# Optimization experiments

Hardware: AMD Instinct MI355X
Metric: run time of the kernel (lower is better)

The kernel has to match this reference:

```python
import jax, jax.numpy as jnp
import numpy as np

H = 1.0                 # grid spacing (init kwarg h)
SRC = (48, 48, 48)      # source grid index = round((x,y,z)/h)
N_ITER = 288
BIG = 1e5               # large-but-finite 'infinity' (keeps gradients NaN-free)


def _godunov_step(u, f):
    """One Jacobi-parallel Godunov upwind update of |grad u| = f on a cubic grid."""
    up = jnp.pad(u, 1, constant_values=BIG)
    # upwind neighbor minima along each axis
    a = jnp.minimum(up[:-2, 1:-1, 1:-1], up[2:, 1:-1, 1:-1])
    b = jnp.minimum(up[1:-1, :-2, 1:-1], up[1:-1, 2:, 1:-1])
    c = jnp.minimum(up[1:-1, 1:-1, :-2], up[1:-1, 1:-1, 2:])
    # sort (a,b,c) -> lo <= mid <= hi
    lo = jnp.minimum(jnp.minimum(a, b), c)
    hi = jnp.maximum(jnp.maximum(a, b), c)
    mid = a + b + c - lo - hi
    fh = f * H
    # 1D candidate
    u1 = lo + fh
    # 2D candidate: (lo+mid+sqrt(2 fh^2 - (lo-mid)^2))/2, guarded sqrt
    d2 = 2.0 * fh * fh - (lo - mid) ** 2
    u2 = jnp.where(d2 > 0, 0.5 * (lo + mid + jnp.sqrt(jnp.where(d2 > 0, d2, 1.0))), BIG)
    # 3D candidate: root of 3 t^2 - 2 s t + (q - fh^2) = 0
    s = lo + mid + hi
    d3 = s * s - 3.0 * (lo * lo + mid * mid + hi * hi - fh * fh)
    u3 = jnp.where(d3 > 0, (s + jnp.sqrt(jnp.where(d3 > 0, d3, 1.0))) / 3.0, BIG)
    cand = jnp.where(u1 <= mid, u1, jnp.where(u2 <= hi, u2, u3))
    un = jnp.minimum(u, cand)          # monotone update (causality)
    return un.at[SRC].set(0.0)         # pin source travel time


def setup_inputs() -> dict:
    key = jax.random.key(0)
    # slowness field, bounded away from zero (velocities in [2/3, 2])
    f = 0.5 + jax.random.uniform(key, (96, 96, 96), dtype=jnp.float32)
    return {"f": f}


def reference(f):
    u0 = jnp.full(f.shape, BIG, dtype=f.dtype).at[SRC].set(0.0)
    step = jax.checkpoint(lambda u, _: (_godunov_step(u, f), None))
    u, _ = jax.lax.scan(step, u0, None, length=N_ITER)
    return u
```

## Files before the change

kernel.cpp:

```cpp
#include <hip/hip_runtime.h>


#define N   96
#define N2  (96 * 96)
#define N3  (96 * 96 * 96)
#define BIGV 1e5f
#define SRC_IDX (48 * N2 + 48 * N + 48)

__global__ __launch_bounds__(256) void eik_init(float* __restrict__ u) {
    int idx = blockIdx.x * 256 + threadIdx.x;
    u[idx] = (idx == SRC_IDX) ? 0.0f : BIGV;
}

__global__ __launch_bounds__(256) void eik_step(const float* __restrict__ u,
                                                const float* __restrict__ f,
                                                float* __restrict__ un) {
    int idx = blockIdx.x * 256 + threadIdx.x;
    int k = idx % N;
    int t = idx / N;
    int j = t % N;
    int i = t / N;

    float uc = u[idx];

    float xm = (i > 0)     ? u[idx - N2] : BIGV;
    float xp = (i < N - 1) ? u[idx + N2] : BIGV;
    float ym = (j > 0)     ? u[idx - N]  : BIGV;
    float yp = (j < N - 1) ? u[idx + N]  : BIGV;
    float zm = (k > 0)     ? u[idx - 1]  : BIGV;
    float zp = (k < N - 1) ? u[idx + 1]  : BIGV;

    float a = fminf(xm, xp);
    float b = fminf(ym, yp);
    float c = fminf(zm, zp);

    float lo  = fminf(fminf(a, b), c);
    float hi  = fmaxf(fmaxf(a, b), c);
    float mid = a + b + c - lo - hi;

    float fh = f[idx];

    float u1 = lo + fh;

    float dlm = lo - mid;
    float d2  = 2.0f * fh * fh - dlm * dlm;
    float u2  = (d2 > 0.0f) ? 0.5f * (lo + mid + sqrtf(d2)) : BIGV;

    float s  = lo + mid + hi;
    float q  = lo * lo + mid * mid + hi * hi - fh * fh;
    float d3 = s * s - 3.0f * q;
    float u3 = (d3 > 0.0f) ? (s + sqrtf(d3)) / 3.0f : BIGV;

    float cand = (u1 <= mid) ? u1 : ((u2 <= hi) ? u2 : u3);
    float unv  = fminf(uc, cand);

    if (idx == SRC_IDX) unv = 0.0f;
    un[idx] = unv;
}

extern "C" void kernel_launch(void* const* d_in, const int* in_sizes, int n_in,
                              void* d_out, int out_size, void* d_ws, size_t ws_size,
                              hipStream_t stream) {
    const float* f = (const float*)d_in[0];
    float* A = (float*)d_out;
    float* B = (float*)d_ws;

    const int nblk = N3 / 256;

    eik_init<<<nblk, 256, 0, stream>>>(A);

    for (int it = 0; it < 288; ++it) {
        const float* src = (it & 1) ? B : A;
        float*       dst = (it & 1) ? A : B;
        eik_step<<<nblk, 256, 0, stream>>>(src, f, dst);
    }
}
```

Before: 1.937 ms.

## Fuse four Jacobi sweeps per launch with LDS temporal blocking and halos

Each block loads a 12^3 tile plus a 4-cell halo into shared memory and performs four Godunov sweeps in LDS with shrinking valid regions before writing the tile back. This cuts kernel launches and global memory round-trips by a factor of four. It also skips the quadratic solve when all neighbors are still at the 'infinity' value. The trade-off is redundant halo computation and a large shared-memory footprint that limits occupancy.

```diff
diff --git a/kernel.cpp b/kernel.cpp
--- a/kernel.cpp
+++ b/kernel.cpp
@@ -1,61 +1,113 @@
 #include <hip/hip_runtime.h>
 
 
-#define N   96
-#define N2  (96 * 96)
-#define N3  (96 * 96 * 96)
+#define N    96
+#define N2   (96 * 96)
+#define N3   (96 * 96 * 96)
 #define BIGV 1e5f
-#define SRC_IDX (48 * N2 + 48 * N + 48)
+#define SRC_IDX ((48 * N + 48) * N + 48)
+
+#define TS   12
+#define S    4
+#define IN   (TS + 2 * S)
+#define IN2  (IN * IN)
+#define IN3  (IN * IN * IN)
+#define NT   (N / TS)
+#define NSTEPS_TOTAL 288
+#define NDISP (NSTEPS_TOTAL / S)
 
 __global__ __launch_bounds__(256) void eik_init(float* __restrict__ u) {
     int idx = blockIdx.x * 256 + threadIdx.x;
     u[idx] = (idx == SRC_IDX) ? 0.0f : BIGV;
 }
 
-__global__ __launch_bounds__(256) void eik_step(const float* __restrict__ u,
-                                                const float* __restrict__ f,
-                                                float* __restrict__ un) {
-    int idx = blockIdx.x * 256 + threadIdx.x;
-    int k = idx % N;
-    int t = idx / N;
-    int j = t % N;
-    int i = t / N;
+template <int R, int O>
+__device__ __forceinline__ void substep(const float* __restrict__ src,
+                                        float* __restrict__ dst,
+                                        const float* __restrict__ f,
+                                        int gx0, int gy0, int gz0) {
+    constexpr int R2 = R * R;
+    constexpr int R3 = R * R * R;
+    for (int idx = threadIdx.x; idx < R3; idx += 256) {
+        int lz  = idx / R2 + O;
+        int rem = idx % R2;
+        int ly  = rem / R + O;
+        int lx  = rem % R + O;
+        int li  = (lz * IN + ly) * IN + lx;
 
-    float uc = u[idx];
+        int gx = gx0 + lx, gy = gy0 + ly, gz = gz0 + lz;
+        bool inside = ((unsigned)gx < N) && ((unsigned)gy < N) && ((unsigned)gz < N);
+        if (!inside) { dst[li] = BIGV; continue; }
 
-    float xm = (i > 0)     ? u[idx - N2] : BIGV;
-    float xp = (i < N - 1) ? u[idx + N2] : BIGV;
-    float ym = (j > 0)     ? u[idx - N]  : BIGV;
-    float yp = (j < N - 1) ? u[idx + N]  : BIGV;
-    float zm = (k > 0)     ? u[idx - 1]  : BIGV;
-    float zp = (k < N - 1) ? u[idx + 1]  : BIGV;
+        float uc = src[li];
+        float a  = fminf(src[li - IN2], src[li + IN2]);
+        float b  = fminf(src[li - IN],  src[li + IN]);
+        float c  = fminf(src[li - 1],   src[li + 1]);
+        float lo = fminf(fminf(a, b), c);
 
-    float a = fminf(xm, xp);
-    float b = fminf(ym, yp);
-    float c = fminf(zm, zp);
+        int gidx = (gz * N + gy) * N + gx;
+        float v;
+        if (lo >= BIGV) {
+            v = uc;
+        } else {
+            float hi  = fmaxf(fmaxf(a, b), c);
+            float mid = a + b + c - lo - hi;
+            float fh  = f[gidx];
 
-    float lo  = fminf(fminf(a, b), c);
-    float hi  = fmaxf(fmaxf(a, b), c);
-    float mid = a + b + c - lo - hi;
+            float u1  = lo + fh;
+            float dlm = lo - mid;
+            float d2  = 2.0f * fh * fh - dlm * dlm;
+            float u2  = (d2 > 0.0f) ? 0.5f * (lo + mid + sqrtf(d2)) : BIGV;
 
-    float fh = f[idx];
+            float s  = lo + mid + hi;
+            float qq = lo * lo + mid * mid + hi * hi - fh * fh;
+            float d3 = s * s - 3.0f * qq;
+            float u3 = (d3 > 0.0f) ? (s + sqrtf(d3)) / 3.0f : BIGV;
 
-    float u1 = lo + fh;
+            float cand = (u1 <= mid) ? u1 : ((u2 <= hi) ? u2 : u3);
+            v = fminf(uc, cand);
+        }
+        if (gidx == SRC_IDX) v = 0.0f;
+        dst[li] = v;
+    }
+}
 
-    float dlm = lo - mid;
-    float d2  = 2.0f * fh * fh - dlm * dlm;
-    float u2  = (d2 > 0.0f) ? 0.5f * (lo + mid + sqrtf(d2)) : BIGV;
+__global__ __launch_bounds__(256) void eik_fused4(const float* __restrict__ u,
+                                                  const float* __restrict__ f,
+                                                  float* __restrict__ un) {
+    __shared__ float su[2][IN3];
 
-    float s  = lo + mid + hi;
-    float q  = lo * lo + mid * mid + hi * hi - fh * fh;
-    float d3 = s * s - 3.0f * q;
-    float u3 = (d3 > 0.0f) ? (s + sqrtf(d3)) / 3.0f : BIGV;
+    int bx = blockIdx.x % NT;
+    int by = (blockIdx.x / NT) % NT;
+    int bz = blockIdx.x / (NT * NT);
+    int gx0 = bx * TS - S;
+    int gy0 = by * TS - S;
+    int gz0 = bz * TS - S;
 
-    float cand = (u1 <= mid) ? u1 : ((u2 <= hi) ? u2 : u3);
-    float unv  = fminf(uc, cand);
+    for (int idx = threadIdx.x; idx < IN3; idx += 256) {
+        int lz  = idx / IN2;
+        int rem = idx % IN2;
+        int ly  = rem / IN;
+        int lx  = rem % IN;
+        int gx = gx0 + lx, gy = gy0 + ly, gz = gz0 + lz;
+        bool inside = ((unsigned)gx < N) && ((unsigned)gy < N) && ((unsigned)gz < N);
+        su[0][idx] = inside ? u[(gz * N + gy) * N + gx] : BIGV;
+    }
+    __syncthreads();
 
-    if (idx == SRC_IDX) unv = 0.0f;
-    un[idx] = unv;
+    substep<18, 1>(su[0], su[1], f, gx0, gy0, gz0); __syncthreads();
+    substep<16, 2>(su[1], su[0], f, gx0, gy0, gz0); __syncthreads();
+    substep<14, 3>(su[0], su[1], f, gx0, gy0, gz0); __syncthreads();
+    substep<12, 4>(su[1], su[0], f, gx0, gy0, gz0); __syncthreads();
+
+    for (int idx = threadIdx.x; idx < TS * TS * TS; idx += 256) {
+        int lz  = idx / (TS * TS) + S;
+        int rem = idx % (TS * TS);
+        int ly  = rem / TS + S;
+        int lx  = rem % TS + S;
+        int gx = gx0 + lx, gy = gy0 + ly, gz = gz0 + lz;
+        un[(gz * N + gy) * N + gx] = su[0][(lz * IN + ly) * IN + lx];
+    }
 }
 
 extern "C" void kernel_launch(void* const* d_in, const int* in_sizes, int n_in,
@@ -65,13 +117,12 @@
     float* A = (float*)d_out;
     float* B = (float*)d_ws;
 
-    const int nblk = N3 / 256;
+    eik_init<<<N3 / 256, 256, 0, stream>>>(A);
 
-    eik_init<<<nblk, 256, 0, stream>>>(A);
-
-    for (int it = 0; it < 288; ++it) {
-        const float* src = (it & 1) ? B : A;
-        float*       dst = (it & 1) ? A : B;
-        eik_step<<<nblk, 256, 0, stream>>>(src, f, dst);
+    const int nblk = NT * NT * NT;
+    for (int d = 0; d < NDISP; ++d) {
+        const float* src = (d & 1) ? B : A;
+        float*       dst = (d & 1) ? A : B;
+        eik_fused4<<<nblk, 256, 0, stream>>>(src, f, dst);
     }
 }
```

Result: slower. 3.102 ms (+60.1%).

## Replace global Jacobi sweeps with tiled fast-iterative in-shared-memory Gauss-Seidel solver

Applied to the files above, without the earlier changes.

Swaps the 288 global Jacobi launches for 40 launches of a block-tiled solver. Each 16^3 tile loads into shared memory and runs alternating-direction Gauss-Seidel sweeps until nothing changes, and per-tile activity flags skip tiles with no active neighbours. The aim is to cut launch count and global memory traffic and to converge in far fewer passes. The cost is a change in numerical semantics: Gauss-Seidel in place instead of Jacobi, fixed iteration caps, and in-place updates shared across tiles. The result may differ from the reference, which is a fixed 288-step Jacobi iteration.

```diff
diff --git a/kernel.cpp b/kernel.cpp
--- a/kernel.cpp
+++ b/kernel.cpp
@@ -1,77 +1,177 @@
 #include <hip/hip_runtime.h>
 
 
-#define N   96
-#define N2  (96 * 96)
-#define N3  (96 * 96 * 96)
-#define BIGV 1e5f
-#define SRC_IDX (48 * N2 + 48 * N + 48)
+#define N      96
+#define BIGV   1e5f
+#define SRC_IDX ((48 * N + 48) * N + 48)
 
-__global__ __launch_bounds__(256) void eik_init(float* __restrict__ u) {
+#define TS     16
+#define NT     (N / TS)
+#define NTILES (NT * NT * NT)
+#define IN     (TS + 2)
+#define IN2    (IN * IN)
+#define IN3    (IN * IN * IN)
+#define TS3    (TS * TS * TS)
+#define KMAX   40
+#define CHK    2
+#define NDISP  40
+#define SRC_TILE (3 * NT * NT + 3 * NT + 3)
+
+__global__ __launch_bounds__(256) void eik_init(float* __restrict__ u,
+                                                int* __restrict__ flagsA) {
     int idx = blockIdx.x * 256 + threadIdx.x;
     u[idx] = (idx == SRC_IDX) ? 0.0f : BIGV;
+    if (blockIdx.x == 0 && threadIdx.x < NTILES)
+        flagsA[threadIdx.x] = (threadIdx.x == SRC_TILE) ? 1 : 0;
 }
 
-__global__ __launch_bounds__(256) void eik_step(const float* __restrict__ u,
-                                                const float* __restrict__ f,
-                                                float* __restrict__ un) {
-    int idx = blockIdx.x * 256 + threadIdx.x;
-    int k = idx % N;
-    int t = idx / N;
-    int j = t % N;
-    int i = t / N;
+__device__ __forceinline__ float god_update(float zn, float xm, float xp,
+                                            float ym, float yp,
+                                            float fh, float uc) {
+    float b = fminf(xm, xp);
+    float c = fminf(ym, yp);
+    float a = zn;
+    float lo = fminf(fminf(a, b), c);
+    if (lo >= BIGV || lo >= uc) return uc;
 
-    float uc = u[idx];
-
-    float xm = (i > 0)     ? u[idx - N2] : BIGV;
-    float xp = (i < N - 1) ? u[idx + N2] : BIGV;
-    float ym = (j > 0)     ? u[idx - N]  : BIGV;
-    float yp = (j < N - 1) ? u[idx + N]  : BIGV;
-    float zm = (k > 0)     ? u[idx - 1]  : BIGV;
-    float zp = (k < N - 1) ? u[idx + 1]  : BIGV;
-
-    float a = fminf(xm, xp);
-    float b = fminf(ym, yp);
-    float c = fminf(zm, zp);
-
-    float lo  = fminf(fminf(a, b), c);
     float hi  = fmaxf(fmaxf(a, b), c);
     float mid = a + b + c - lo - hi;
+    float u1  = lo + fh;
+    float cand;
+    if (u1 <= mid) {
+        cand = u1;
+    } else {
+        float dlm = lo - mid;
+        float d2  = 2.0f * fh * fh - dlm * dlm;
+        float u2  = (d2 > 0.0f) ? 0.5f * (lo + mid + sqrtf(d2)) : BIGV;
+        if (u2 <= hi) {
+            cand = u2;
+        } else {
+            float s  = lo + mid + hi;
+            float qq = lo * lo + mid * mid + hi * hi - fh * fh;
+            float d3 = s * s - 3.0f * qq;
+            cand = (d3 > 0.0f) ? (s + sqrtf(d3)) / 3.0f : BIGV;
+        }
+    }
+    return fminf(uc, cand);
+}
 
-    float fh = f[idx];
+__global__ __launch_bounds__(256) void eik_fim(float* __restrict__ u,
+                                               const float* __restrict__ f,
+                                               const int* __restrict__ fin,
+                                               int* __restrict__ fout) {
+    __shared__ float su[IN3];
+    __shared__ float sf[TS3];
+    __shared__ int s_act;
+    __shared__ int s_chg;
 
-    float u1 = lo + fh;
+    const int bid = blockIdx.x;
+    const int tx = threadIdx.x, ty = threadIdx.y;
+    const int tid = ty * TS + tx;
+    const int bx = bid % NT, by = (bid / NT) % NT, bz = bid / (NT * NT);
 
-    float dlm = lo - mid;
-    float d2  = 2.0f * fh * fh - dlm * dlm;
-    float u2  = (d2 > 0.0f) ? 0.5f * (lo + mid + sqrtf(d2)) : BIGV;
+    if (tid == 0) {
+        int a = fin[bid];
+        if (bx > 0)      a |= fin[bid - 1];
+        if (bx < NT - 1) a |= fin[bid + 1];
+        if (by > 0)      a |= fin[bid - NT];
+        if (by < NT - 1) a |= fin[bid + NT];
+        if (bz > 0)      a |= fin[bid - NT * NT];
+        if (bz < NT - 1) a |= fin[bid + NT * NT];
+        s_act = a;
+        s_chg = 0;
+    }
+    __syncthreads();
+    if (!s_act) { if (tid == 0) fout[bid] = 0; return; }
 
-    float s  = lo + mid + hi;
-    float q  = lo * lo + mid * mid + hi * hi - fh * fh;
-    float d3 = s * s - 3.0f * q;
-    float u3 = (d3 > 0.0f) ? (s + sqrtf(d3)) / 3.0f : BIGV;
+    const int gx0 = bx * TS - 1, gy0 = by * TS - 1, gz0 = bz * TS - 1;
 
-    float cand = (u1 <= mid) ? u1 : ((u2 <= hi) ? u2 : u3);
-    float unv  = fminf(uc, cand);
+    for (int idx = tid; idx < IN3; idx += 256) {
+        int lz = idx / IN2, rem = idx - lz * IN2;
+        int ly = rem / IN,  lx = rem - ly * IN;
+        int gx = gx0 + lx, gy = gy0 + ly, gz = gz0 + lz;
+        bool ins = ((unsigned)gx < N) & ((unsigned)gy < N) & ((unsigned)gz < N);
+        su[idx] = ins ? u[(gz * N + gy) * N + gx] : BIGV;
+    }
+    {
+        const int fx0 = bx * TS, fy0 = by * TS, fz0 = bz * TS;
+        for (int idx = tid; idx < TS3; idx += 256) {
+            int lz = idx >> 8, ly = (idx >> 4) & 15, lx = idx & 15;
+            sf[idx] = f[((fz0 + lz) * N + fy0 + ly) * N + fx0 + lx];
+        }
+    }
+    __syncthreads();
 
-    if (idx == SRC_IDX) unv = 0.0f;
-    un[idx] = unv;
+    const int coff = (ty + 1) * IN + (tx + 1);
+    int any_change = 0;
+
+    for (int s = 0; s < KMAX; ++s) {
+        int changed = 0;
+        if ((s & 1) == 0) {
+            float um = su[coff];
+            float uc = su[IN2 + coff];
+            #pragma unroll
+            for (int zi = 1; zi <= TS; ++zi) {
+                const int li = zi * IN2 + coff;
+                float up = su[li + IN2];
+                float xm = su[li - 1],  xp = su[li + 1];
+                float ym = su[li - IN], yp = su[li + IN];
+                float fh = sf[(zi - 1) * (TS * TS) + tid];
+                float v  = god_update(fminf(um, up), xm, xp, ym, yp, fh, uc);
+                if (v < uc) { su[li] = v; changed = 1; }
+                um = v; uc = up;
+            }
+        } else {
+            float up = su[(TS + 1) * IN2 + coff];
+            float uc = su[TS * IN2 + coff];
+            #pragma unroll
+            for (int zi = TS; zi >= 1; --zi) {
+                const int li = zi * IN2 + coff;
+                float um = su[li - IN2];
+                float xm = su[li - 1],  xp = su[li + 1];
+                float ym = su[li - IN], yp = su[li + IN];
+                float fh = sf[(zi - 1) * (TS * TS) + tid];
+                float v  = god_update(fminf(um, up), xm, xp, ym, yp, fh, uc);
+                if (v < uc) { su[li] = v; changed = 1; }
+                up = v; uc = um;
+            }
+        }
+        if (changed) s_chg = 1;
+        if ((s & (CHK - 1)) == (CHK - 1)) {
+            __syncthreads();
+            int c = s_chg;
+            __syncthreads();
+            if (tid == 0) s_chg = 0;
+            __syncthreads();
+            if (!c) break;
+            any_change = 1;
+        }
+    }
+    __syncthreads();
+
+    if (any_change) {
+        #pragma unroll
+        for (int zi = 1; zi <= TS; ++zi) {
+            int gz = gz0 + zi;
+            u[(gz * N + (gy0 + ty + 1)) * N + (gx0 + tx + 1)] = su[zi * IN2 + coff];
+        }
+    }
+    if (tid == 0) fout[bid] = any_change;
 }
 
 extern "C" void kernel_launch(void* const* d_in, const int* in_sizes, int n_in,
                               void* d_out, int out_size, void* d_ws, size_t ws_size,
                               hipStream_t stream) {
     const float* f = (const float*)d_in[0];
-    float* A = (float*)d_out;
-    float* B = (float*)d_ws;
+    float* u = (float*)d_out;
+    int* flagsA = (int*)d_ws;
+    int* flagsB = flagsA + 256;
 
-    const int nblk = N3 / 256;
+    eik_init<<<(N * N * N) / 256, 256, 0, stream>>>(u, flagsA);
 
-    eik_init<<<nblk, 256, 0, stream>>>(A);
-
-    for (int it = 0; it < 288; ++it) {
-        const float* src = (it & 1) ? B : A;
-        float*       dst = (it & 1) ? A : B;
-        eik_step<<<nblk, 256, 0, stream>>>(src, f, dst);
+    for (int d = 0; d < NDISP; ++d) {
+        const int* fi = (d & 1) ? flagsB : flagsA;
+        int*       fo = (d & 1) ? flagsA : flagsB;
+        eik_fim<<<NTILES, dim3(TS, TS), 0, stream>>>(u, f, fi, fo);
     }
 }
```

New measurement: 4.952 ms. 156% more time.
